# Kernel tuning notes

Measured on AMD Instinct MI355X. Metric: run time of the kernel, lower is better.

The kernel has to match this reference:

```python
import jax, jax.numpy as jnp
import numpy as np

T, B, F, H, O = 512, 1024, 16, 32, 8  # seq_len, batch, input_size, hidden, classes


def setup_inputs() -> dict:
    key = jax.random.key(0)
    ks = jax.random.split(key, 11)
    s = 1.0 / np.sqrt(H)  # PyTorch LSTM/Linear uniform init scale
    u = lambda k, shp: jax.random.uniform(k, shp, jnp.float32, -s, s)
    return {
        "x": jax.random.normal(ks[0], (T, B, F), jnp.float32),
        "W_ih_f": u(ks[1], (4 * H, F)),
        "W_hh_f": u(ks[2], (4 * H, H)),
        "b_f": u(ks[3], (4 * H,)),  # combined b_ih + b_hh
        "W_ih_b": u(ks[4], (4 * H, F)),
        "W_hh_b": u(ks[5], (4 * H, H)),
        "b_b": u(ks[6], (4 * H,)),
        "W_fc_h": u(ks[7], (O, 2 * H)),
        "b_fc_h": u(ks[8], (O,)),
        "W_fc_o": jax.random.uniform(ks[9], (O, B * O), jnp.float32, -1 / np.sqrt(B * O), 1 / np.sqrt(B * O)),
        "b_fc_o": u(ks[10], (O,)),
    }


def _lstm_final_hidden(x, W_ih, W_hh, b):
    """Run one LSTM direction over x:(T,B,F); return final hidden h:(B,H)."""
    h_dim = W_hh.shape[1]
    # precompute input contribution for all timesteps: (T, B, 4H)
    gates_x = jnp.einsum('tbf,gf->tbg', x, W_ih) + b

    def step(carry, gx):
        h, c = carry
        g = gx + h @ W_hh.T  # (B, 4H), PyTorch gate order i,f,g,o
        i, f, gg, o = jnp.split(g, 4, axis=-1)
        c = jax.nn.sigmoid(f) * c + jax.nn.sigmoid(i) * jnp.tanh(gg)
        h = jax.nn.sigmoid(o) * jnp.tanh(c)
        return (h, c), None

    bsz = x.shape[1]
    init = (jnp.zeros((bsz, h_dim), x.dtype), jnp.zeros((bsz, h_dim), x.dtype))
    (h, _), _ = jax.lax.scan(step, init, gates_x)
    return h


def reference(x, W_ih_f, W_hh_f, b_f, W_ih_b, W_hh_b, b_b,
              W_fc_h, b_fc_h, W_fc_o, b_fc_o):
    h_fwd = _lstm_final_hidden(x, W_ih_f, W_hh_f, b_f)          # hidden_state[-2]
    h_bwd = _lstm_final_hidden(x[::-1], W_ih_b, W_hh_b, b_b)    # hidden_state[-1]
    hidden = jnp.concatenate([h_fwd, h_bwd], axis=1)            # (B, 2H)
    hidden_fc = hidden @ W_fc_h.T + b_fc_h                      # (B, O)
    flat = hidden_fc.reshape(-1)                                # (B*O,) == flat_dim
    out = W_fc_o @ flat + b_fc_o                                # (O,)
    return jax.nn.softmax(out)
```

## Files before the change

kernel.cpp:

```cpp
#include <hip/hip_runtime.h>

#define TT 512
#define BB 1024
#define FF 16
#define HH 32
#define OO 8
#define CH 16
#define NC (TT / CH)
#define NG 128

typedef _Float16 f16;
typedef f16 v2h __attribute__((ext_vector_type(2)));
typedef f16 v4h __attribute__((ext_vector_type(4)));
typedef f16 v8h __attribute__((ext_vector_type(8)));
typedef float f32x4 __attribute__((ext_vector_type(4)));
typedef int   v2i  __attribute__((ext_vector_type(2)));

__device__ __forceinline__ float rcp_fast(float x) { return __builtin_amdgcn_rcpf(x); }
__device__ __forceinline__ float sigm2(float y) {
    return rcp_fast(1.0f + __builtin_amdgcn_exp2f(-y));
}
__device__ __forceinline__ float fdot2(v2h a, v2h b, float c) {
    return __builtin_amdgcn_fdot2(a, b, c, false);
}
__device__ __forceinline__ v2h i2h(int s) { return __builtin_bit_cast(v2h, s); }

__device__ __forceinline__ float xhalf_swap(float v) {
#if __has_builtin(__builtin_amdgcn_permlane32_swap)
    int pi = __float_as_int(v);
    v2i sw = __builtin_amdgcn_permlane32_swap(pi, pi, false, false);
    return __int_as_float(sw.x);
#else
    return __shfl_xor(v, 32);
#endif
}

__global__ __launch_bounds__(64, 2)
void lstm_seq_kernel(const float* __restrict__ x,
                     const float* __restrict__ Wih_f, const float* __restrict__ Whh_f,
                     const float* __restrict__ b_f,
                     const float* __restrict__ Wih_b, const float* __restrict__ Whh_b,
                     const float* __restrict__ b_b,
                     float* __restrict__ hidden)
{
    const int bid  = blockIdx.x;
    const int dir  = bid >> 10;
    const int bb   = bid & (BB - 1);
    const int lane = threadIdx.x;
    const int hi   = lane >> 5;
    const int kk   = lane & 31;

    const float* __restrict__ Wih  = dir ? Wih_b : Wih_f;
    const float* __restrict__ Whh  = dir ? Whh_b : Whh_f;
    const float* __restrict__ bias = dir ? b_b   : b_f;

    const float LOG2E = 1.4426950408889634f;
    const float L2E2  = 2.0f * LOG2E;

    const int r0 = kk + hi * HH;
    const int r1 = r0 + 2 * HH;
    const float sc0 = LOG2E;
    const float sc1 = hi ? LOG2E : L2E2;
    const float pm = hi ? 1.0f : 2.0f;
    const float pa = hi ? 0.0f : -1.0f;

    v2h w0h[HH / 2], w1h[HH / 2];
#pragma unroll
    for (int q = 0; q < HH / 4; ++q) {
        float4 a = ((const float4*)(Whh + r0 * HH))[q];
        w0h[2*q]   = (v2h){(f16)(a.x * sc0), (f16)(a.y * sc0)};
        w0h[2*q+1] = (v2h){(f16)(a.z * sc0), (f16)(a.w * sc0)};
        float4 b2 = ((const float4*)(Whh + r1 * HH))[q];
        w1h[2*q]   = (v2h){(f16)(b2.x * sc1), (f16)(b2.y * sc1)};
        w1h[2*q+1] = (v2h){(f16)(b2.z * sc1), (f16)(b2.w * sc1)};
    }
    const float pb0 = bias[r0] * sc0;
    const float pb1 = bias[r1] * sc1;

    v8h aw[8];
#pragma unroll
    for (int T = 0; T < 8; ++T) {
        v8h t = {(f16)0,(f16)0,(f16)0,(f16)0,(f16)0,(f16)0,(f16)0,(f16)0};
        if (lane < 32) {
            const int gate = T * 16 + (lane & 15);
            const float sc = (gate >= 64 && gate < 96) ? L2E2 : LOG2E;
            const float* wrow = Wih + gate * FF + (lane >> 4) * 8;
#pragma unroll
            for (int j = 0; j < 8; ++j) t[j] = (f16)(wrow[j] * sc);
        }
        aw[T] = t;
    }

    __shared__ __align__(16) f16   xsb[2 * CH * FF];
    __shared__ __align__(16) float gxb[2 * CH * NG];

    const int sl = lane >> 2;
    const int wl = lane & 3;
    const int t0 = dir ? (TT - 1 - sl) : sl;
    const float* xp = x + (size_t)t0 * (BB * FF) + (size_t)bb * FF + wl * 4;
    const ptrdiff_t dstep = (dir ? -(ptrdiff_t)CH : (ptrdiff_t)CH) * (BB * FF);

    const int mst = lane & 15;
    const int mq  = (lane >> 4) * 4;
    const int mxr = (mst & 7) << 2;

    {
        float4 f0 = *(const float4*)xp;
        *(v4h*)(xsb + sl * FF + wl * 4) =
            (v4h){(f16)f0.x, (f16)f0.y, (f16)f0.z, (f16)f0.w};
    }
    xp += dstep;
    __syncthreads();
    {
        v8h bx = {(f16)0,(f16)0,(f16)0,(f16)0,(f16)0,(f16)0,(f16)0,(f16)0};
        if (lane < 32)
            bx = *(const v8h*)(xsb + (lane & 15) * FF + (lane >> 4) * 8);
        float* gw = gxb + mst * NG;
#pragma unroll
        for (int T = 0; T < 8; ++T) {
            f32x4 acc = __builtin_amdgcn_mfma_f32_16x16x32_f16(
                aw[T], bx, (f32x4){0.f, 0.f, 0.f, 0.f}, 0, 0, 0);
            *(f32x4*)(gw + ((mq + T * 16) ^ mxr)) = acc;
        }
    }
    float4 nf = *(const float4*)xp;
    xp += dstep;
    __syncthreads();

    float c = 0.0f, h = 0.0f;
    int hs[HH / 2];
#pragma unroll
    for (int m = 0; m < HH / 2; ++m) hs[m] = 0;

    for (int ci = 0; ci < NC; ++ci) {
        const int bufc = ci & 1;
        if (ci + 1 < NC) {
            const int bufn = bufc ^ 1;
            *(v4h*)(xsb + bufn * (CH * FF) + sl * FF + wl * 4) =
                (v4h){(f16)nf.x, (f16)nf.y, (f16)nf.z, (f16)nf.w};
            v8h bx = {(f16)0,(f16)0,(f16)0,(f16)0,(f16)0,(f16)0,(f16)0,(f16)0};
            if (lane < 32)
                bx = *(const v8h*)(xsb + bufn * (CH * FF) + (lane & 15) * FF + (lane >> 4) * 8);
            float* gw = gxb + bufn * (CH * NG) + mst * NG;
#pragma unroll
            for (int T = 0; T < 8; ++T) {
                f32x4 acc = __builtin_amdgcn_mfma_f32_16x16x32_f16(
                    aw[T], bx, (f32x4){0.f, 0.f, 0.f, 0.f}, 0, 0, 0);
                *(f32x4*)(gw + ((mq + T * 16) ^ mxr)) = acc;
            }
            if (ci + 2 < NC) { nf = *(const float4*)xp; xp += dstep; }
        }

        const float* gxc = gxb + bufc * (CH * NG);
#pragma unroll
        for (int tt = 0; tt < CH; ++tt) {
            const int xm = (tt & 7) << 2;
            const float gx0 = gxc[tt * NG + (r0 ^ xm)];
            const float gx1 = gxc[tt * NG + (r1 ^ xm)];

            float B0 = fdot2(i2h(hs[0]), w0h[0], pb0);
            float B1 = fdot2(i2h(hs[0]), w1h[0], pb1);
            float C0 = fdot2(i2h(hs[8]), w0h[8], gx0);
            float C1 = fdot2(i2h(hs[8]), w1h[8], gx1);
#pragma unroll
            for (int j = 1; j < 8; ++j) {
                B0 = fdot2(i2h(hs[j]),     w0h[j],     B0);
                B1 = fdot2(i2h(hs[j]),     w1h[j],     B1);
                C0 = fdot2(i2h(hs[8 + j]), w0h[8 + j], C0);
                C1 = fdot2(i2h(hs[8 + j]), w1h[8 + j], C1);
            }
            const float g0 = B0 + C0;
            const float g1 = B1 + C1;

            const float s0 = sigm2(g0);
            const float s1 = fmaf(sigm2(g1), pm, pa);
            const float prod = s0 * s1;

            const float recv = xhalf_swap(prod);
            c = fmaf(s0, c, recv);
            const float th = fmaf(2.0f, sigm2(L2E2 * c), -1.0f);
            h = s1 * th;

            const int hn = __builtin_amdgcn_mov_dpp(__float_as_int(h),
                                                    0xB1, 0xF, 0xF, true);
            auto pk = __builtin_amdgcn_cvt_pkrtz(h, __int_as_float(hn));
            const int pki = __builtin_bit_cast(int, pk);
#pragma unroll
            for (int m = 0; m < HH / 2; ++m)
                hs[m] = __builtin_amdgcn_readlane(pki, 32 + 2 * m);
        }
        __syncthreads();
    }

    if (hi) hidden[(size_t)bb * 64 + dir * HH + kk] = h;
}

__global__ __launch_bounds__(256)
void fc_partial_kernel(const float* __restrict__ hidden,
                       const float* __restrict__ Wfh, const float* __restrict__ bfh,
                       const float* __restrict__ Wfo,
                       float* __restrict__ partials)
{
    __shared__ float wsh[OO * 64];
    const int tid = threadIdx.x;
    for (int i = tid; i < OO * 64; i += 256) wsh[i] = Wfh[i];
    __syncthreads();

    const int r   = tid >> 3;
    const int o   = tid & 7;
    const int row = blockIdx.x * 32 + r;

    const float* hrow = hidden + (size_t)row * 64;
    float acc = bfh[o];
#pragma unroll
    for (int j = 0; j < 64; ++j) acc += hrow[j] * wsh[o * 64 + j];

    const int fidx = blockIdx.x * 256 + tid;

    float pv[OO];
#pragma unroll
    for (int o2 = 0; o2 < OO; ++o2) pv[o2] = Wfo[(size_t)o2 * (BB * OO) + fidx] * acc;

    __shared__ float red[4][OO];
#pragma unroll
    for (int o2 = 0; o2 < OO; ++o2) {
        float v = pv[o2];
        for (int off = 32; off > 0; off >>= 1) v += __shfl_down(v, off);
        if ((tid & 63) == 0) red[tid >> 6][o2] = v;
    }
    __syncthreads();
    if (tid < OO) {
        partials[blockIdx.x * OO + tid] =
            red[0][tid] + red[1][tid] + red[2][tid] + red[3][tid];
    }
}

__global__ void finalize_kernel(const float* __restrict__ partials,
                                const float* __restrict__ bfo,
                                float* __restrict__ out)
{
    __shared__ float s[OO];
    const int tid = threadIdx.x;
    if (tid < OO) {
        float acc = bfo[tid];
        for (int b = 0; b < 32; ++b) acc += partials[b * OO + tid];
        s[tid] = acc;
    }
    __syncthreads();
    if (tid == 0) {
        float m = s[0];
        for (int i = 1; i < OO; ++i) m = fmaxf(m, s[i]);
        float e[OO], sum = 0.0f;
        for (int i = 0; i < OO; ++i) { e[i] = expf(s[i] - m); sum += e[i]; }
        for (int i = 0; i < OO; ++i) out[i] = e[i] / sum;
    }
}

extern "C" void kernel_launch(void* const* d_in, const int* in_sizes, int n_in,
                              void* d_out, int out_size, void* d_ws, size_t ws_size,
                              hipStream_t stream) {
    const float* x     = (const float*)d_in[0];
    const float* Wih_f = (const float*)d_in[1];
    const float* Whh_f = (const float*)d_in[2];
    const float* b_f   = (const float*)d_in[3];
    const float* Wih_b = (const float*)d_in[4];
    const float* Whh_b = (const float*)d_in[5];
    const float* b_b   = (const float*)d_in[6];
    const float* Wfh   = (const float*)d_in[7];
    const float* bfh   = (const float*)d_in[8];
    const float* Wfo   = (const float*)d_in[9];
    const float* bfo   = (const float*)d_in[10];

    float* hidden   = (float*)d_ws;
    float* partials = hidden + (size_t)BB * 64;

    lstm_seq_kernel<<<2 * BB, 64, 0, stream>>>(x, Wih_f, Whh_f, b_f,
                                               Wih_b, Whh_b, b_b, hidden);
    fc_partial_kernel<<<32, 256, 0, stream>>>(hidden, Wfh, bfh, Wfo, partials);
    finalize_kernel<<<1, 64, 0, stream>>>(partials, bfo, (float*)d_out);
}
```

Before: 177.5 us.

## Compute LSTM recurrent matvec with MFMA and broadcast hidden state via LDS

Each timestep's recurrent product h·W_hh now runs as eight 16x16x32 f16 MFMA instructions, where it used to be chains of packed fdot2 over register-held weight rows. The hidden state is passed between steps through a small LDS buffer, replacing the earlier readlane broadcast. Each lane now picks its own i/f/g/o gate values out of the MFMA outputs and computes the cell update itself, so the cross-half permlane swap is gone. The aim is a shorter serial dependency chain per step. In exchange, every step adds an LDS write/read round trip and MFMA latency, wastes MFMA columns on a vector that is replicated across them, and duplicates the gate math across non-owner lanes.

```diff
diff --git a/kernel.cpp b/kernel.cpp
--- a/kernel.cpp
+++ b/kernel.cpp
@@ -10,29 +10,13 @@
 #define NG 128
 
 typedef _Float16 f16;
-typedef f16 v2h __attribute__((ext_vector_type(2)));
 typedef f16 v4h __attribute__((ext_vector_type(4)));
 typedef f16 v8h __attribute__((ext_vector_type(8)));
 typedef float f32x4 __attribute__((ext_vector_type(4)));
-typedef int   v2i  __attribute__((ext_vector_type(2)));
 
 __device__ __forceinline__ float rcp_fast(float x) { return __builtin_amdgcn_rcpf(x); }
 __device__ __forceinline__ float sigm2(float y) {
     return rcp_fast(1.0f + __builtin_amdgcn_exp2f(-y));
-}
-__device__ __forceinline__ float fdot2(v2h a, v2h b, float c) {
-    return __builtin_amdgcn_fdot2(a, b, c, false);
-}
-__device__ __forceinline__ v2h i2h(int s) { return __builtin_bit_cast(v2h, s); }
-
-__device__ __forceinline__ float xhalf_swap(float v) {
-#if __has_builtin(__builtin_amdgcn_permlane32_swap)
-    int pi = __float_as_int(v);
-    v2i sw = __builtin_amdgcn_permlane32_swap(pi, pi, false, false);
-    return __int_as_float(sw.x);
-#else
-    return __shfl_xor(v, 32);
-#endif
 }
 
 __global__ __launch_bounds__(64, 2)
@@ -47,8 +31,12 @@
     const int dir  = bid >> 10;
     const int bb   = bid & (BB - 1);
     const int lane = threadIdx.x;
-    const int hi   = lane >> 5;
-    const int kk   = lane & 31;
+
+    const int  rsel  = lane & 3;
+    const int  kh    = (lane >> 3) & 1;
+    const int  grp   = lane >> 4;
+    const int  u     = 4 * grp + rsel + 16 * kh;
+    const bool owner = ((lane & 4) == 0);
 
     const float* __restrict__ Wih  = dir ? Wih_b : Wih_f;
     const float* __restrict__ Whh  = dir ? Whh_b : Whh_f;
@@ -57,27 +45,18 @@
     const float LOG2E = 1.4426950408889634f;
     const float L2E2  = 2.0f * LOG2E;
 
-    const int r0 = kk + hi * HH;
-    const int r1 = r0 + 2 * HH;
-    const float sc0 = LOG2E;
-    const float sc1 = hi ? LOG2E : L2E2;
-    const float pm = hi ? 1.0f : 2.0f;
-    const float pa = hi ? 0.0f : -1.0f;
-
-    v2h w0h[HH / 2], w1h[HH / 2];
-#pragma unroll
-    for (int q = 0; q < HH / 4; ++q) {
-        float4 a = ((const float4*)(Whh + r0 * HH))[q];
-        w0h[2*q]   = (v2h){(f16)(a.x * sc0), (f16)(a.y * sc0)};
-        w0h[2*q+1] = (v2h){(f16)(a.z * sc0), (f16)(a.w * sc0)};
-        float4 b2 = ((const float4*)(Whh + r1 * HH))[q];
-        w1h[2*q]   = (v2h){(f16)(b2.x * sc1), (f16)(b2.y * sc1)};
-        w1h[2*q+1] = (v2h){(f16)(b2.z * sc1), (f16)(b2.w * sc1)};
-    }
-    const float pb0 = bias[r0] * sc0;
-    const float pb1 = bias[r1] * sc1;
-
-    v8h aw[8];
+    v8h awh[8];
+#pragma unroll
+    for (int T = 0; T < 8; ++T) {
+        const float sc = (T == 4 || T == 5) ? L2E2 : LOG2E;
+        const float* wrow = Whh + (T * 16 + (lane & 15)) * HH + grp * 8;
+        v8h t;
+#pragma unroll
+        for (int j = 0; j < 8; ++j) t[j] = (f16)(wrow[j] * sc);
+        awh[T] = t;
+    }
+
+    v8h awx[8];
 #pragma unroll
     for (int T = 0; T < 8; ++T) {
         v8h t = {(f16)0,(f16)0,(f16)0,(f16)0,(f16)0,(f16)0,(f16)0,(f16)0};
@@ -88,11 +67,17 @@
 #pragma unroll
             for (int j = 0; j < 8; ++j) t[j] = (f16)(wrow[j] * sc);
         }
-        aw[T] = t;
-    }
+        awx[T] = t;
+    }
+
+    float pb[4];
+#pragma unroll
+    for (int cc = 0; cc < 4; ++cc)
+        pb[cc] = bias[u + 32 * cc] * ((cc == 2) ? L2E2 : LOG2E);
 
     __shared__ __align__(16) f16   xsb[2 * CH * FF];
     __shared__ __align__(16) float gxb[2 * CH * NG];
+    __shared__ __align__(16) f16   hbuf[HH];
 
     const int sl = lane >> 2;
     const int wl = lane & 3;
@@ -110,6 +95,7 @@
             (v4h){(f16)f0.x, (f16)f0.y, (f16)f0.z, (f16)f0.w};
     }
     xp += dstep;
+    if (lane < HH) hbuf[lane] = (f16)0.0f;
     __syncthreads();
     {
         v8h bx = {(f16)0,(f16)0,(f16)0,(f16)0,(f16)0,(f16)0,(f16)0,(f16)0};
@@ -119,7 +105,7 @@
 #pragma unroll
         for (int T = 0; T < 8; ++T) {
             f32x4 acc = __builtin_amdgcn_mfma_f32_16x16x32_f16(
-                aw[T], bx, (f32x4){0.f, 0.f, 0.f, 0.f}, 0, 0, 0);
+                awx[T], bx, (f32x4){0.f, 0.f, 0.f, 0.f}, 0, 0, 0);
             *(f32x4*)(gw + ((mq + T * 16) ^ mxr)) = acc;
         }
     }
@@ -128,9 +114,6 @@
     __syncthreads();
 
     float c = 0.0f, h = 0.0f;
-    int hs[HH / 2];
-#pragma unroll
-    for (int m = 0; m < HH / 2; ++m) hs[m] = 0;
 
     for (int ci = 0; ci < NC; ++ci) {
         const int bufc = ci & 1;
@@ -145,7 +128,7 @@
 #pragma unroll
             for (int T = 0; T < 8; ++T) {
                 f32x4 acc = __builtin_amdgcn_mfma_f32_16x16x32_f16(
-                    aw[T], bx, (f32x4){0.f, 0.f, 0.f, 0.f}, 0, 0, 0);
+                    awx[T], bx, (f32x4){0.f, 0.f, 0.f, 0.f}, 0, 0, 0);
                 *(f32x4*)(gw + ((mq + T * 16) ^ mxr)) = acc;
             }
             if (ci + 2 < NC) { nf = *(const float4*)xp; xp += dstep; }
@@ -154,45 +137,51 @@
         const float* gxc = gxb + bufc * (CH * NG);
 #pragma unroll
         for (int tt = 0; tt < CH; ++tt) {
+            const v8h bh = *(const v8h*)(hbuf + grp * 8);
+
+            f32x4 acc[8];
+#pragma unroll
+            for (int T = 0; T < 8; ++T)
+                acc[T] = __builtin_amdgcn_mfma_f32_16x16x32_f16(
+                    awh[T], bh, (f32x4){0.f, 0.f, 0.f, 0.f}, 0, 0, 0);
+
             const int xm = (tt & 7) << 2;
-            const float gx0 = gxc[tt * NG + (r0 ^ xm)];
-            const float gx1 = gxc[tt * NG + (r1 ^ xm)];
-
-            float B0 = fdot2(i2h(hs[0]), w0h[0], pb0);
-            float B1 = fdot2(i2h(hs[0]), w1h[0], pb1);
-            float C0 = fdot2(i2h(hs[8]), w0h[8], gx0);
-            float C1 = fdot2(i2h(hs[8]), w1h[8], gx1);
-#pragma unroll
-            for (int j = 1; j < 8; ++j) {
-                B0 = fdot2(i2h(hs[j]),     w0h[j],     B0);
-                B1 = fdot2(i2h(hs[j]),     w1h[j],     B1);
-                C0 = fdot2(i2h(hs[8 + j]), w0h[8 + j], C0);
-                C1 = fdot2(i2h(hs[8 + j]), w1h[8 + j], C1);
+            float gb[4];
+#pragma unroll
+            for (int cc = 0; cc < 4; ++cc)
+                gb[cc] = gxc[tt * NG + ((u + 32 * cc) ^ xm)] + pb[cc];
+
+            float e[4];
+#pragma unroll
+            for (int cc = 0; cc < 4; ++cc) {
+                const f32x4 ta = acc[2 * cc];
+                const f32x4 tb = acc[2 * cc + 1];
+                const float a0 = (lane & 2) ? ((lane & 1) ? ta[3] : ta[2])
+                                            : ((lane & 1) ? ta[1] : ta[0]);
+                const float a1 = (lane & 2) ? ((lane & 1) ? tb[3] : tb[2])
+                                            : ((lane & 1) ? tb[1] : tb[0]);
+                e[cc] = kh ? a1 : a0;
             }
-            const float g0 = B0 + C0;
-            const float g1 = B1 + C1;
-
-            const float s0 = sigm2(g0);
-            const float s1 = fmaf(sigm2(g1), pm, pa);
-            const float prod = s0 * s1;
-
-            const float recv = xhalf_swap(prod);
-            c = fmaf(s0, c, recv);
+
+            const float gi = e[0] + gb[0];
+            const float gf = e[1] + gb[1];
+            const float gg = e[2] + gb[2];
+            const float go = e[3] + gb[3];
+
+            const float si = sigm2(gi);
+            const float sf = sigm2(gf);
+            const float tg = fmaf(2.0f, sigm2(gg), -1.0f);
+            const float so = sigm2(go);
+            c = fmaf(sf, c, si * tg);
             const float th = fmaf(2.0f, sigm2(L2E2 * c), -1.0f);
-            h = s1 * th;
-
-            const int hn = __builtin_amdgcn_mov_dpp(__float_as_int(h),
-                                                    0xB1, 0xF, 0xF, true);
-            auto pk = __builtin_amdgcn_cvt_pkrtz(h, __int_as_float(hn));
-            const int pki = __builtin_bit_cast(int, pk);
-#pragma unroll
-            for (int m = 0; m < HH / 2; ++m)
-                hs[m] = __builtin_amdgcn_readlane(pki, 32 + 2 * m);
+            h = so * th;
+
+            if (owner) hbuf[u] = (f16)h;
         }
         __syncthreads();
     }
 
-    if (hi) hidden[(size_t)bb * 64 + dir * HH + kk] = h;
+    if (owner) hidden[(size_t)bb * 64 + dir * HH + u] = h;
 }
 
 __global__ __launch_bounds__(256)
```

Measured after the change: 217.3 us. +22.4%, slower.
